# Performance work log

Measured on AMD Instinct MI355X. Metric: run time of the kernel, lower is better.

Reference implementation:

```python
import jax, jax.numpy as jnp
import numpy as np

RATIO = 4

def positional_encoding(d_model, max_len, w_s):
    # w_s: (B,) per-example frequency warp. pe[b, p, 0::2]=sin, pe[b, p, 1::2]=cos
    pos = jnp.arange(max_len, dtype=jnp.float32)                      # (L,)
    div = jnp.power(10000.0, jnp.arange(0, d_model, 2, dtype=jnp.float32) / d_model)  # (d/2,)
    ang = w_s[:, None, None] * pos[None, :, None] / div[None, None, :]  # (B, L, d/2)
    pe = jnp.stack([jnp.sin(ang), jnp.cos(ang)], axis=-1)             # (B, L, d/2, 2)
    return pe.reshape(w_s.shape[0], max_len, d_model)

def setup_inputs() -> dict:
    key = jax.random.key(0)
    ks = jax.random.split(key, 6)
    B, Tds, L, D = 32, 2048, 512, 256
    q = jax.random.normal(ks[0], (B, Tds, D), dtype=jnp.float32)
    k = jax.random.normal(ks[1], (B, L, D), dtype=jnp.float32)
    v = jax.random.normal(ks[2], (B, L, D), dtype=jnp.float32)
    w_compress = jax.random.normal(ks[3], (D // RATIO, D), dtype=jnp.float32) * (D ** -0.5)
    text_lengths = jax.random.randint(ks[4], (B,), L // 2, L + 1).at[0].set(L)
    mel_lengths = jax.random.randint(ks[5], (B,), (Tds * RATIO) // 2, Tds * RATIO + 1).at[0].set(Tds * RATIO)
    return {"q": q, "k": k, "v": v, "w_compress": w_compress,
            "text_lengths": text_lengths, "mel_lengths": mel_lengths}

def reference(q, k, v, w_compress, text_lengths, mel_lengths):
    B, Tds, D = q.shape
    L = k.shape[1]
    # padding masks (True = padded)
    text_mask = jnp.arange(L)[None, :] >= text_lengths[:, None]            # (B, L)
    mel_mask_ds = jnp.arange(Tds)[None, :] >= (mel_lengths // RATIO)[:, None]  # (B, Tds)
    # positional encodings
    q = q + positional_encoding(D, Tds, jnp.ones((B,), dtype=jnp.float32))
    w_s = mel_lengths.astype(jnp.float32) / RATIO / text_lengths.astype(jnp.float32)
    k = k + positional_encoding(D, L, w_s)
    q = q * (float(D) ** -0.5)
    # scores + masked softmax over text axis
    scores = jnp.einsum('btd,bld->btl', q, k)                              # (B, Tds, L)
    scores = jnp.where(text_mask[:, None, :], -jnp.inf, scores)
    align = jax.nn.softmax(scores, axis=-1)
    align = jnp.where(mel_mask_ds[:, :, None], 0.0, align)
    # hard argmax one-hot, straight-through blend
    idx = jnp.argmax(align, axis=-1)                                       # (B, Tds)
    align_oh = jax.nn.one_hot(idx, L, dtype=align.dtype)
    align_oh = jnp.where(mel_mask_ds[:, :, None], 0.0, align_oh)
    blend = align + jax.lax.stop_gradient(align_oh - align)
    attn = jnp.einsum('btl,bld->btd', blend, v)                            # (B, Tds, D)
    # Compress (Linear D -> D//ratio, no bias) then transpose(1,2)
    out = jnp.einsum('btd,cd->bct', attn, w_compress)                      # (B, D//ratio, Tds)
    return out, align
```

## Files before the change

kernel.cpp:

```cpp
#include <hip/hip_runtime.h>
#include <math.h>

#define NB  32
#define TDS 2048
#define LL  512
#define DD  256
#define DC  64
#define GAP_THR 4e-4f

typedef __attribute__((ext_vector_type(8)))  short short8;
typedef __attribute__((ext_vector_type(16))) float f32x16;
typedef __attribute__((ext_vector_type(4)))  float f32x4;

__device__ __forceinline__ unsigned short f2bf(float x) {
    union { float f; unsigned u; } v; v.f = x;
    unsigned r = v.u + 0x7fffu + ((v.u >> 16) & 1u);
    return (unsigned short)(r >> 16);
}
__device__ __forceinline__ float bf2f(unsigned short h) {
    union { unsigned u; float f; } v; v.u = ((unsigned)h) << 16;
    return v.f;
}
__device__ __forceinline__ void gll16(const void* g, void* l) {
    __builtin_amdgcn_global_load_lds(
        (const __attribute__((address_space(1))) void*)g,
        (__attribute__((address_space(3))) void*)l, 16, 0, 0);
}
__device__ __forceinline__ int swz3(int x) { return (x & 7) ^ ((x >> 3) & 7); }


__global__ void peq_kernel(float* __restrict__ peq, int* __restrict__ cnt) {
    int idx = blockIdx.x * 256 + threadIdx.x;
    if (idx == 0) cnt[0] = 0;
    int t = idx >> 8;
    int d = idx & 255;
    int i = d >> 1;
    double invdiv = exp((double)i * (-9.210340371976184 / 128.0));
    double ang = (double)t * invdiv;
    double s, c;
    sincos(ang, &s, &c);
    peq[idx] = (float)((d & 1) ? c : s);
}

__global__ __launch_bounds__(256)
void pek_kernel(const float* __restrict__ k,
                const int* __restrict__ text_lengths,
                const int* __restrict__ mel_lengths,
                char* __restrict__ hi_base,
                char* __restrict__ lo_base) {
    __shared__ double invdiv[128];
    const int tid = threadIdx.x;
    if (tid < 128) invdiv[tid] = exp((double)tid * (-9.210340371976184 / 128.0));
    __syncthreads();
    int f = blockIdx.x * 256 + tid;
    int b = f >> 14;
    int r = f & 16383;
    int ks = r >> 11;
    int rr = r & 2047;
    int lt = rr >> 9;
    int r2 = rr & 511;
    int c  = r2 >> 2;
    int ch = r2 & 3;
    int l  = lt * 128 + c;
    int kk = ks * 32 + ch * 8;
    const float* kr = k + ((size_t)(b * LL + l)) * DD + kk;
    float4 kv0 = *(const float4*)(kr);
    float4 kv1 = *(const float4*)(kr + 4);
    float kv[8] = {kv0.x, kv0.y, kv0.z, kv0.w, kv1.x, kv1.y, kv1.z, kv1.w};
    double wsd = ((double)mel_lengths[b] * 0.25) / (double)text_lengths[b];
    double base_ang = wsd * (double)l;
    unsigned short h[8], lo8[8];
#pragma unroll
    for (int jj = 0; jj < 4; ++jj) {
        int i = (kk >> 1) + jj;
        double ang = base_ang * invdiv[i];
        double n = rint(ang * 0.15915494309189535);
        double red = fma(n, -6.283185307179586, ang);
        float sn, cs;
        sincosf((float)red, &sn, &cs);
        float e0 = kv[2 * jj] + sn;
        float e1 = kv[2 * jj + 1] + cs;
        h[2 * jj]       = f2bf(e0);
        h[2 * jj + 1]   = f2bf(e1);
        lo8[2 * jj]     = f2bf(e0 - bf2f(h[2 * jj]));
        lo8[2 * jj + 1] = f2bf(e1 - bf2f(h[2 * jj + 1]));
    }
    size_t off = (size_t)b * 262144 + (size_t)(ks * 4 + lt) * 8192
               + (size_t)((c * 64 + ch * 16) ^ (swz3(c) << 4));
    uint4 hv, lv;
    hv.x = h[0] | ((unsigned)h[1] << 16); hv.y = h[2] | ((unsigned)h[3] << 16);
    hv.z = h[4] | ((unsigned)h[5] << 16); hv.w = h[6] | ((unsigned)h[7] << 16);
    lv.x = lo8[0] | ((unsigned)lo8[1] << 16); lv.y = lo8[2] | ((unsigned)lo8[3] << 16);
    lv.z = lo8[4] | ((unsigned)lo8[5] << 16); lv.w = lo8[6] | ((unsigned)lo8[7] << 16);
    *(uint4*)(hi_base + off) = hv;
    *(uint4*)(lo_base + off) = lv;
}

__global__ __launch_bounds__(256, 4)
void score_kernel(const float* __restrict__ q,
                  const float* __restrict__ peq,
                  const char* __restrict__ kps_hi,
                  const char* __restrict__ kps_lo,
                  const int* __restrict__ text_lengths,
                  const int* __restrict__ mel_lengths,
                  float* __restrict__ align_out,
                  int* __restrict__ idx_out,
                  int* __restrict__ flag_cnt,
                  int* __restrict__ flags) {
    __shared__ alignas(16) char smB[2 * 16384];
    __shared__ alignas(16) char smA[2 * 4096];

    struct Epi {
        float v1[4][32]; int i1[4][32]; float v2[4][32];
        float S[4][32];  float M[32];
    };
    Epi* ep = (Epi*)smA;

    const int wgid = blockIdx.x;
    const int xcd = wgid & 7, loc = wgid >> 3;
    const int nid = xcd * 256 + loc;
    const int b  = nid >> 6;
    const int t0 = (nid & 63) << 5;

    const int tid = threadIdx.x;
    const int wn = tid >> 6, lane = tid & 63;
    const int c31 = lane & 31, hi5 = lane >> 5;
    const int tlen = text_lengths[b];
    const int melq = mel_lengths[b] >> 2;

    const char* khb = kps_hi + (size_t)b * 262144;
    const char* klb = kps_lo + (size_t)b * 262144;

    f32x16 acc[4];
#pragma unroll
    for (int lt = 0; lt < 4; ++lt)
#pragma unroll
        for (int rg = 0; rg < 16; ++rg) acc[lt][rg] = 0.f;

    const int cB = wn * 32 + c31;
    int aoff[2], boff[2];
#pragma unroll
    for (int kh = 0; kh < 2; ++kh) {
        aoff[kh] = (c31 * 64 + kh * 32 + hi5 * 16) ^ (swz3(c31) << 4);
        boff[kh] = (cB  * 64 + kh * 32 + hi5 * 16) ^ (swz3(cB)  << 4);
    }

    const int sr  = tid >> 3;
    const int sk0 = (tid & 7) * 4;
    const float* qrow = q   + ((size_t)(b * TDS + t0 + sr)) * DD + sk0;
    const float* prow = peq + ((size_t)(t0 + sr)) * DD + sk0;
    const int awaddr = (sr * 64 + sk0 * 2) ^ (swz3(sr) << 4);

#define STAGEB(dbuf, tidx)                                                      \
    {                                                                           \
        const size_t toff = (size_t)(tidx) * 8192 + tid * 16;                   \
        char* dh = smB + (dbuf) * 16384 + tid * 16;                             \
        char* dl = dh + 8192;                                                   \
        gll16(khb + toff, dh); gll16(khb + toff + 4096, dh + 4096);             \
        gll16(klb + toff, dl); gll16(klb + toff + 4096, dl + 4096);             \
    }
#define AWRITE(abufi)                                                           \
    {                                                                           \
        float a0 = (qv4.x + pv4.x) * 0.0625f, a1 = (qv4.y + pv4.y) * 0.0625f;   \
        float a2 = (qv4.z + pv4.z) * 0.0625f, a3 = (qv4.w + pv4.w) * 0.0625f;   \
        unsigned short h0 = f2bf(a0), h1 = f2bf(a1), h2 = f2bf(a2), h3 = f2bf(a3); \
        ushort4 hv = {h0, h1, h2, h3};                                          \
        ushort4 lv = {f2bf(a0 - bf2f(h0)), f2bf(a1 - bf2f(h1)),                 \
                      f2bf(a2 - bf2f(h2)), f2bf(a3 - bf2f(h3))};                \
        *(ushort4*)(smA + (abufi) * 4096 + awaddr) = hv;                        \
        *(ushort4*)(smA + (abufi) * 4096 + 2048 + awaddr) = lv;                 \
    }
#define MFMA6(LT, BUF)                                                          \
    {                                                                           \
        const char* bb = smB + (BUF) * 16384;                                   \
        short8 bh0 = *(const short8*)(bb + boff[0]);                            \
        short8 bl0 = *(const short8*)(bb + 8192 + boff[0]);                     \
        short8 bh1 = *(const short8*)(bb + boff[1]);                            \
        short8 bl1 = *(const short8*)(bb + 8192 + boff[1]);                     \
        acc[LT] = __builtin_amdgcn_mfma_f32_32x32x16_bf16(ah0, bh0, acc[LT], 0, 0, 0); \
        acc[LT] = __builtin_amdgcn_mfma_f32_32x32x16_bf16(ah0, bl0, acc[LT], 0, 0, 0); \
        acc[LT] = __builtin_amdgcn_mfma_f32_32x32x16_bf16(al0, bh0, acc[LT], 0, 0, 0); \
        acc[LT] = __builtin_amdgcn_mfma_f32_32x32x16_bf16(ah1, bh1, acc[LT], 0, 0, 0); \
        acc[LT] = __builtin_amdgcn_mfma_f32_32x32x16_bf16(ah1, bl1, acc[LT], 0, 0, 0); \
        acc[LT] = __builtin_amdgcn_mfma_f32_32x32x16_bf16(al1, bh1, acc[LT], 0, 0, 0); \
    }

    float4 qv4 = *(const float4*)(qrow);
    float4 pv4 = *(const float4*)(prow);
    AWRITE(0)
    STAGEB(0, 0)
    __syncthreads();

    for (int ks = 0; ks < 8; ++ks) {
        const char* abase = smA + (ks & 1) * 4096;
        short8 ah0 = *(const short8*)(abase + aoff[0]);
        short8 ah1 = *(const short8*)(abase + aoff[1]);
        short8 al0 = *(const short8*)(abase + 2048 + aoff[0]);
        short8 al1 = *(const short8*)(abase + 2048 + aoff[1]);
        const int p0 = ks * 4;
        STAGEB(1, p0 + 1)
        MFMA6(0, 0)
        __syncthreads();
        STAGEB(0, p0 + 2)
        if (ks < 7) {
            qv4 = *(const float4*)(qrow + (ks + 1) * 32);
            pv4 = *(const float4*)(prow + (ks + 1) * 32);
        }
        MFMA6(1, 1)
        __syncthreads();
        STAGEB(1, p0 + 3)
        MFMA6(2, 0)
        __syncthreads();
        if (ks < 7) STAGEB(0, p0 + 4)
        MFMA6(3, 1)
        if (ks < 7) AWRITE((ks + 1) & 1)
        __syncthreads();
    }
#undef STAGEB
#undef AWRITE
#undef MFMA6

    const float NEGINF = -__builtin_inff();
#pragma unroll
    for (int lt = 0; lt < 4; ++lt) {
        int col = lt * 128 + cB;
        if (col >= tlen) {
#pragma unroll
            for (int rg = 0; rg < 16; ++rg) acc[lt][rg] = NEGINF;
        }
    }
    float v1[16]; int i1[16]; float v2[16];
#pragma unroll
    for (int rg = 0; rg < 16; ++rg) {
        v1[rg] = acc[0][rg]; i1[rg] = cB; v2[rg] = NEGINF;
#pragma unroll
        for (int lt = 1; lt < 4; ++lt) {
            float v = acc[lt][rg]; int col = lt * 128 + cB;
            if (v > v1[rg]) { v2[rg] = v1[rg]; v1[rg] = v; i1[rg] = col; }
            else if (v > v2[rg]) v2[rg] = v;
        }
    }
#pragma unroll
    for (int off = 1; off <= 16; off <<= 1) {
#pragma unroll
        for (int rg = 0; rg < 16; ++rg) {
            float ov1 = __shfl_xor(v1[rg], off, 64);
            int   oi1 = __shfl_xor(i1[rg], off, 64);
            float ov2 = __shfl_xor(v2[rg], off, 64);
            if (ov1 > v1[rg]) { v2[rg] = fmaxf(v1[rg], ov2); v1[rg] = ov1; i1[rg] = oi1; }
            else if (ov1 < v1[rg]) { v2[rg] = fmaxf(v2[rg], ov1); }
            else { i1[rg] = min(i1[rg], oi1); v2[rg] = v1[rg]; }
        }
    }
    if (c31 == 0) {
#pragma unroll
        for (int rg = 0; rg < 16; ++rg) {
            int r32 = (rg & 3) + 8 * (rg >> 2) + 4 * hi5;
            ep->v1[wn][r32] = v1[rg]; ep->i1[wn][r32] = i1[rg]; ep->v2[wn][r32] = v2[rg];
        }
    }
    __syncthreads();
    {
        const int r32 = c31;
        float V1 = ep->v1[0][r32]; int I1 = ep->i1[0][r32]; float V2 = ep->v2[0][r32];
#pragma unroll
        for (int w = 1; w < 4; ++w) {
            float cv1 = ep->v1[w][r32]; int ci1 = ep->i1[w][r32]; float cv2 = ep->v2[w][r32];
            if (cv1 > V1) { V2 = fmaxf(V1, cv2); V1 = cv1; I1 = ci1; }
            else if (cv1 < V1) { V2 = fmaxf(V2, cv1); }
            else { V2 = V1; }
        }
        if (wn == 0 && hi5 == 0) {
            int t = t0 + r32;
            idx_out[b * TDS + t] = I1;
            if (t < melq && (V1 - V2) < GAP_THR) {
                int pos = atomicAdd(flag_cnt, 1);
                flags[pos] = (b << 11) | t;
            }
            ep->M[r32] = V1;
        }
    }
    __syncthreads();
    float ssum[16];
#pragma unroll
    for (int rg = 0; rg < 16; ++rg) {
        int r32 = (rg & 3) + 8 * (rg >> 2) + 4 * hi5;
        float M = ep->M[r32];
        float s = 0.f;
#pragma unroll
        for (int lt = 0; lt < 4; ++lt) {
            float p = __expf(acc[lt][rg] - M);
            acc[lt][rg] = p; s += p;
        }
        ssum[rg] = s;
    }
#pragma unroll
    for (int off = 1; off <= 16; off <<= 1)
#pragma unroll
        for (int rg = 0; rg < 16; ++rg) ssum[rg] += __shfl_xor(ssum[rg], off, 64);
    if (c31 == 0) {
#pragma unroll
        for (int rg = 0; rg < 16; ++rg) {
            int r32 = (rg & 3) + 8 * (rg >> 2) + 4 * hi5;
            ep->S[wn][r32] = ssum[rg];
        }
    }
    __syncthreads();
#pragma unroll
    for (int rg = 0; rg < 16; ++rg) {
        int r32 = (rg & 3) + 8 * (rg >> 2) + 4 * hi5;
        int t = t0 + r32;
        float denom = ep->S[0][r32] + ep->S[1][r32] + ep->S[2][r32] + ep->S[3][r32];
        float sc = (t < melq) ? (1.0f / denom) : 0.f;
        size_t obase = ((size_t)(b * TDS + t)) * LL + cB;
#pragma unroll
        for (int lt = 0; lt < 4; ++lt)
            __builtin_nontemporal_store(acc[lt][rg] * sc, align_out + obase + lt * 128);
    }
}

__global__ __launch_bounds__(256)
void refine_kernel(const float* __restrict__ q,
                   const float* __restrict__ k,
                   const int* __restrict__ text_lengths,
                   const int* __restrict__ mel_lengths,
                   const int* __restrict__ flags,
                   const int* __restrict__ flag_cnt,
                   int* __restrict__ idx_out) {
    __shared__ double qd[DD];
    __shared__ double invdiv[128];
    __shared__ double rbest[4];
    __shared__ int    ribest[4];
    const int tid = threadIdx.x;
    if (tid < 128)
        invdiv[tid] = 1.0 / pow(10000.0, (double)tid * (1.0 / 128.0));
    const int cnt = flag_cnt[0];
    for (int r = blockIdx.x; r < cnt; r += gridDim.x) {
        const int code = flags[r];
        const int b = code >> 11, t = code & 2047;
        const int tlen = text_lengths[b];
        const double ws = ((double)mel_lengths[b] * 0.25) / (double)text_lengths[b];
        __syncthreads();
        {
            const int d = tid, i = d >> 1;
            double ang = (double)t * invdiv[i];
            double sn, cs;
            sincos(ang, &sn, &cs);
            qd[d] = ((double)q[((size_t)b * TDS + t) * DD + d] + ((d & 1) ? cs : sn)) * 0.0625;
        }
        __syncthreads();
        double best = -1.0e300; int bi = 0x7fffffff;
        for (int p = 0; p < 2; ++p) {
            const int l = tid + p * 256;
            if (l < tlen) {
                const float* kr = k + ((size_t)b * LL + l) * DD;
                const double wl = ws * (double)l;
                double sacc = 0.0;
                for (int i = 0; i < 128; ++i) {
                    double ang = wl * invdiv[i];
                    double sn, cs;
                    sincos(ang, &sn, &cs);
                    sacc += ((double)kr[2 * i]     + sn) * qd[2 * i];
                    sacc += ((double)kr[2 * i + 1] + cs) * qd[2 * i + 1];
                }
                if (sacc > best || (sacc == best && l < bi)) { best = sacc; bi = l; }
            }
        }
        for (int off = 1; off <= 32; off <<= 1) {
            double ov = __shfl_xor(best, off, 64);
            int   oi = __shfl_xor(bi, off, 64);
            if (ov > best || (ov == best && oi < bi)) { best = ov; bi = oi; }
        }
        const int wv = tid >> 6;
        if ((tid & 63) == 0) { rbest[wv] = best; ribest[wv] = bi; }
        __syncthreads();
        if (tid == 0) {
            double bb = rbest[0]; int ii = ribest[0];
            for (int w = 1; w < 4; ++w)
                if (rbest[w] > bb || (rbest[w] == bb && ribest[w] < ii)) { bb = rbest[w]; ii = ribest[w]; }
            idx_out[b * TDS + t] = ii;
        }
    }
}

__global__ __launch_bounds__(256, 4)
void compress_kernel(const float* __restrict__ v,
                     const float* __restrict__ wc,
                     const int* __restrict__ idx_in,
                     const int* __restrict__ mel_lengths,
                     float* __restrict__ out) {
    __shared__ float Ws[256 * 68];
    __shared__ float Vs[16 * 132];
    __shared__ int   idxs[128];
    const int b   = blockIdx.y;
    const int t0  = blockIdx.x * 128;
    const int tid = threadIdx.x;
    const int melq = mel_lengths[b] >> 2;
    const float* vb = v + (size_t)b * LL * DD;

    if (tid < 128) {
        int t = t0 + tid;
        int ii = idx_in[b * TDS + t];
        idxs[tid] = (t >= melq) ? -1 : ii;
    }
#pragma unroll
    for (int r = 0; r < 16; ++r) {
        int f = tid + r * 256;
        int c = f >> 6;
        int u = f & 63;
        float4 wv = *(const float4*)(wc + (size_t)c * DD + u * 4);
        Ws[(u * 4 + 0) * 68 + c] = wv.x;
        Ws[(u * 4 + 1) * 68 + c] = wv.y;
        Ws[(u * 4 + 2) * 68 + c] = wv.z;
        Ws[(u * 4 + 3) * 68 + c] = wv.w;
    }

    const int tx = tid & 7;
    const int ty = tid >> 3;
    const int tv = tid >> 2;
    const int uv = tid & 3;
    float acc[8][4];
#pragma unroll
    for (int i = 0; i < 8; ++i)
#pragma unroll
        for (int j = 0; j < 4; ++j) acc[i][j] = 0.f;

    for (int ks = 0; ks < 16; ++ks) {
        const int d0 = ks * 16;
        __syncthreads();
#pragma unroll
        for (int p = 0; p < 2; ++p) {
            int t = tv + p * 64;
            int row = idxs[t];
            float4 vv = make_float4(0.f, 0.f, 0.f, 0.f);
            if (row >= 0) vv = *(const float4*)(vb + (size_t)row * DD + d0 + uv * 4);
            Vs[(uv * 4 + 0) * 132 + t] = vv.x;
            Vs[(uv * 4 + 1) * 132 + t] = vv.y;
            Vs[(uv * 4 + 2) * 132 + t] = vv.z;
            Vs[(uv * 4 + 3) * 132 + t] = vv.w;
        }
        __syncthreads();
#pragma unroll
        for (int kk = 0; kk < 16; ++kk) {
            const float* wrow = Ws + (size_t)(d0 + kk) * 68 + tx * 8;
            float4 a0 = *(const float4*)(wrow);
            float4 a1 = *(const float4*)(wrow + 4);
            float4 bb = *(const float4*)(Vs + kk * 132 + ty * 4);
            const float av[8] = {a0.x, a0.y, a0.z, a0.w, a1.x, a1.y, a1.z, a1.w};
            const float bv[4] = {bb.x, bb.y, bb.z, bb.w};
#pragma unroll
            for (int i = 0; i < 8; ++i)
#pragma unroll
                for (int j = 0; j < 4; ++j)
                    acc[i][j] = fmaf(av[i], bv[j], acc[i][j]);
        }
    }
#pragma unroll
    for (int ci = 0; ci < 8; ++ci) {
        int c = tx * 8 + ci;
        f32x4 o = {acc[ci][0], acc[ci][1], acc[ci][2], acc[ci][3]};
        __builtin_nontemporal_store(o, (f32x4*)(out + ((size_t)(b * DC + c)) * TDS + t0 + ty * 4));
    }
}

extern "C" void kernel_launch(void* const* d_in, const int* in_sizes, int n_in,
                              void* d_out, int out_size, void* d_ws, size_t ws_size,
                              hipStream_t stream) {
    const float* q    = (const float*)d_in[0];
    const float* k    = (const float*)d_in[1];
    const float* v    = (const float*)d_in[2];
    const float* wc   = (const float*)d_in[3];
    const int*   text = (const int*)d_in[4];
    const int*   mel  = (const int*)d_in[5];

    float* out   = (float*)d_out;
    float* align = out + (size_t)NB * DC * TDS;

    char*  wsb = (char*)d_ws;
    char*  KPS_HI = wsb;
    char*  KPS_LO = wsb + 8388608;
    float* PEQ = (float*)(wsb + 16777216);
    int*   IDX = (int*)(wsb + 16777216 + 2097152);
    int*   CNT = IDX + (size_t)NB * TDS;
    int*   FLG = CNT + 1;

    hipLaunchKernelGGL(peq_kernel, dim3(TDS * DD / 256), dim3(256), 0, stream, PEQ, CNT);
    hipLaunchKernelGGL(pek_kernel, dim3(NB * LL * 32 / 256), dim3(256), 0, stream,
                       k, text, mel, KPS_HI, KPS_LO);
    hipLaunchKernelGGL(score_kernel, dim3(2048), dim3(256), 0, stream,
                       q, PEQ, KPS_HI, KPS_LO, text, mel, align, IDX, CNT, FLG);
    hipLaunchKernelGGL(refine_kernel, dim3(256), dim3(256), 0, stream,
                       q, k, text, mel, FLG, CNT, IDX);
    hipLaunchKernelGGL(compress_kernel, dim3(TDS / 128, NB), dim3(256), 0, stream,
                       v, wc, IDX, mel, out);
}
```

Measured before the change: 232.4 us.

## Load K fragments directly from global in MFMA layout, drop LDS staging

The precomputed K+PE (bf16 hi/lo) buffer is re-laid out so that each lane's MFMA B fragment can be read straight from global memory with 16-byte loads. The score kernel no longer stages K tiles through LDS or hits per-tile barriers, and it register double-buffers the B fragments instead. The whole Q+PE A tile is converted and written to LDS once up front, and each wave now owns a contiguous 128-column slice. This removes LDS traffic and __syncthreads from the main loop, but makes the K reads depend on L2 and raises register pressure.

```diff
diff --git a/kernel.cpp b/kernel.cpp
--- a/kernel.cpp
+++ b/kernel.cpp
@@ -21,12 +21,6 @@
     union { unsigned u; float f; } v; v.u = ((unsigned)h) << 16;
     return v.f;
 }
-__device__ __forceinline__ void gll16(const void* g, void* l) {
-    __builtin_amdgcn_global_load_lds(
-        (const __attribute__((address_space(1))) void*)g,
-        (__attribute__((address_space(3))) void*)l, 16, 0, 0);
-}
-__device__ __forceinline__ int swz3(int x) { return (x & 7) ^ ((x >> 3) & 7); }
 
 
 __global__ void peq_kernel(float* __restrict__ peq, int* __restrict__ cnt) {
@@ -46,8 +40,7 @@
 void pek_kernel(const float* __restrict__ k,
                 const int* __restrict__ text_lengths,
                 const int* __restrict__ mel_lengths,
-                char* __restrict__ hi_base,
-                char* __restrict__ lo_base) {
+                char* __restrict__ kps) {
     __shared__ double invdiv[128];
     const int tid = threadIdx.x;
     if (tid < 128) invdiv[tid] = exp((double)tid * (-9.210340371976184 / 128.0));
@@ -56,14 +49,15 @@
     int b = f >> 14;
     int r = f & 16383;
     int ks = r >> 11;
-    int rr = r & 2047;
-    int lt = rr >> 9;
-    int r2 = rr & 511;
-    int c  = r2 >> 2;
-    int ch = r2 & 3;
-    int l  = lt * 128 + c;
-    int kk = ks * 32 + ch * 8;
-    const float* kr = k + ((size_t)(b * LL + l)) * DD + kk;
+    int r2 = r & 2047;
+    int cs = r2 >> 7;
+    int r3 = r2 & 127;
+    int kh = r3 >> 6;
+    int g  = (r3 >> 5) & 1;
+    int lane32 = r3 & 31;
+    int l  = cs * 32 + lane32;
+    int k0 = ks * 32 + kh * 16 + g * 8;
+    const float* kr = k + ((size_t)(b * LL + l)) * DD + k0;
     float4 kv0 = *(const float4*)(kr);
     float4 kv1 = *(const float4*)(kr + 4);
     float kv[8] = {kv0.x, kv0.y, kv0.z, kv0.w, kv1.x, kv1.y, kv1.z, kv1.w};
@@ -72,49 +66,46 @@
     unsigned short h[8], lo8[8];
 #pragma unroll
     for (int jj = 0; jj < 4; ++jj) {
-        int i = (kk >> 1) + jj;
+        int i = (k0 >> 1) + jj;
         double ang = base_ang * invdiv[i];
         double n = rint(ang * 0.15915494309189535);
         double red = fma(n, -6.283185307179586, ang);
-        float sn, cs;
-        sincosf((float)red, &sn, &cs);
+        float sn, cs2;
+        sincosf((float)red, &sn, &cs2);
         float e0 = kv[2 * jj] + sn;
-        float e1 = kv[2 * jj + 1] + cs;
+        float e1 = kv[2 * jj + 1] + cs2;
         h[2 * jj]       = f2bf(e0);
         h[2 * jj + 1]   = f2bf(e1);
         lo8[2 * jj]     = f2bf(e0 - bf2f(h[2 * jj]));
         lo8[2 * jj + 1] = f2bf(e1 - bf2f(h[2 * jj + 1]));
     }
-    size_t off = (size_t)b * 262144 + (size_t)(ks * 4 + lt) * 8192
-               + (size_t)((c * 64 + ch * 16) ^ (swz3(c) << 4));
+    size_t off = (size_t)b * 524288 + (size_t)ks * 65536 + (size_t)cs * 4096
+               + kh * 1024 + g * 512 + lane32 * 16;
     uint4 hv, lv;
     hv.x = h[0] | ((unsigned)h[1] << 16); hv.y = h[2] | ((unsigned)h[3] << 16);
     hv.z = h[4] | ((unsigned)h[5] << 16); hv.w = h[6] | ((unsigned)h[7] << 16);
     lv.x = lo8[0] | ((unsigned)lo8[1] << 16); lv.y = lo8[2] | ((unsigned)lo8[3] << 16);
     lv.z = lo8[4] | ((unsigned)lo8[5] << 16); lv.w = lo8[6] | ((unsigned)lo8[7] << 16);
-    *(uint4*)(hi_base + off) = hv;
-    *(uint4*)(lo_base + off) = lv;
+    *(uint4*)(kps + off) = hv;
+    *(uint4*)(kps + off + 2048) = lv;
 }
 
 __global__ __launch_bounds__(256, 4)
 void score_kernel(const float* __restrict__ q,
                   const float* __restrict__ peq,
-                  const char* __restrict__ kps_hi,
-                  const char* __restrict__ kps_lo,
+                  const char* __restrict__ kps,
                   const int* __restrict__ text_lengths,
                   const int* __restrict__ mel_lengths,
                   float* __restrict__ align_out,
                   int* __restrict__ idx_out,
                   int* __restrict__ flag_cnt,
                   int* __restrict__ flags) {
-    __shared__ alignas(16) char smB[2 * 16384];
-    __shared__ alignas(16) char smA[2 * 4096];
-
+    __shared__ alignas(16) char smA[32768];
     struct Epi {
         float v1[4][32]; int i1[4][32]; float v2[4][32];
         float S[4][32];  float M[32];
     };
-    Epi* ep = (Epi*)smA;
+    __shared__ Epi ep;
 
     const int wgid = blockIdx.x;
     const int xcd = wgid & 7, loc = wgid >> 3;
@@ -128,114 +119,104 @@
     const int tlen = text_lengths[b];
     const int melq = mel_lengths[b] >> 2;
 
-    const char* khb = kps_hi + (size_t)b * 262144;
-    const char* klb = kps_lo + (size_t)b * 262144;
+    const char* kpb = kps + (size_t)b * 524288 + (size_t)(hi5 * 512 + c31 * 16);
 
     f32x16 acc[4];
 #pragma unroll
-    for (int lt = 0; lt < 4; ++lt)
-#pragma unroll
-        for (int rg = 0; rg < 16; ++rg) acc[lt][rg] = 0.f;
-
-    const int cB = wn * 32 + c31;
-    int aoff[2], boff[2];
-#pragma unroll
-    for (int kh = 0; kh < 2; ++kh) {
-        aoff[kh] = (c31 * 64 + kh * 32 + hi5 * 16) ^ (swz3(c31) << 4);
-        boff[kh] = (cB  * 64 + kh * 32 + hi5 * 16) ^ (swz3(cB)  << 4);
-    }
-
-    const int sr  = tid >> 3;
-    const int sk0 = (tid & 7) * 4;
-    const float* qrow = q   + ((size_t)(b * TDS + t0 + sr)) * DD + sk0;
-    const float* prow = peq + ((size_t)(t0 + sr)) * DD + sk0;
-    const int awaddr = (sr * 64 + sk0 * 2) ^ (swz3(sr) << 4);
-
-#define STAGEB(dbuf, tidx)                                                      \
+    for (int ci = 0; ci < 4; ++ci)
+#pragma unroll
+        for (int rg = 0; rg < 16; ++rg) acc[ci][rg] = 0.f;
+
+#define BLOAD(dst, ksv, civ)                                                    \
     {                                                                           \
-        const size_t toff = (size_t)(tidx) * 8192 + tid * 16;                   \
-        char* dh = smB + (dbuf) * 16384 + tid * 16;                             \
-        char* dl = dh + 8192;                                                   \
-        gll16(khb + toff, dh); gll16(khb + toff + 4096, dh + 4096);             \
-        gll16(klb + toff, dl); gll16(klb + toff + 4096, dl + 4096);             \
-    }
-#define AWRITE(abufi)                                                           \
+        const char* p = kpb + (ksv) * 65536 + (wn * 4 + (civ)) * 4096;          \
+        dst[0] = *(const short8*)(p);                                           \
+        dst[1] = *(const short8*)(p + 1024);                                    \
+        dst[2] = *(const short8*)(p + 2048);                                    \
+        dst[3] = *(const short8*)(p + 3072);                                    \
+    }
+#define MFMA6(CI, B)                                                            \
     {                                                                           \
-        float a0 = (qv4.x + pv4.x) * 0.0625f, a1 = (qv4.y + pv4.y) * 0.0625f;   \
-        float a2 = (qv4.z + pv4.z) * 0.0625f, a3 = (qv4.w + pv4.w) * 0.0625f;   \
-        unsigned short h0 = f2bf(a0), h1 = f2bf(a1), h2 = f2bf(a2), h3 = f2bf(a3); \
-        ushort4 hv = {h0, h1, h2, h3};                                          \
-        ushort4 lv = {f2bf(a0 - bf2f(h0)), f2bf(a1 - bf2f(h1)),                 \
-                      f2bf(a2 - bf2f(h2)), f2bf(a3 - bf2f(h3))};                \
-        *(ushort4*)(smA + (abufi) * 4096 + awaddr) = hv;                        \
-        *(ushort4*)(smA + (abufi) * 4096 + 2048 + awaddr) = lv;                 \
-    }
-#define MFMA6(LT, BUF)                                                          \
-    {                                                                           \
-        const char* bb = smB + (BUF) * 16384;                                   \
-        short8 bh0 = *(const short8*)(bb + boff[0]);                            \
-        short8 bl0 = *(const short8*)(bb + 8192 + boff[0]);                     \
-        short8 bh1 = *(const short8*)(bb + boff[1]);                            \
-        short8 bl1 = *(const short8*)(bb + 8192 + boff[1]);                     \
-        acc[LT] = __builtin_amdgcn_mfma_f32_32x32x16_bf16(ah0, bh0, acc[LT], 0, 0, 0); \
-        acc[LT] = __builtin_amdgcn_mfma_f32_32x32x16_bf16(ah0, bl0, acc[LT], 0, 0, 0); \
-        acc[LT] = __builtin_amdgcn_mfma_f32_32x32x16_bf16(al0, bh0, acc[LT], 0, 0, 0); \
-        acc[LT] = __builtin_amdgcn_mfma_f32_32x32x16_bf16(ah1, bh1, acc[LT], 0, 0, 0); \
-        acc[LT] = __builtin_amdgcn_mfma_f32_32x32x16_bf16(ah1, bl1, acc[LT], 0, 0, 0); \
-        acc[LT] = __builtin_amdgcn_mfma_f32_32x32x16_bf16(al1, bh1, acc[LT], 0, 0, 0); \
-    }
-
-    float4 qv4 = *(const float4*)(qrow);
-    float4 pv4 = *(const float4*)(prow);
-    AWRITE(0)
-    STAGEB(0, 0)
+        acc[CI] = __builtin_amdgcn_mfma_f32_32x32x16_bf16(ah0, B[0], acc[CI], 0, 0, 0); \
+        acc[CI] = __builtin_amdgcn_mfma_f32_32x32x16_bf16(ah0, B[2], acc[CI], 0, 0, 0); \
+        acc[CI] = __builtin_amdgcn_mfma_f32_32x32x16_bf16(al0, B[0], acc[CI], 0, 0, 0); \
+        acc[CI] = __builtin_amdgcn_mfma_f32_32x32x16_bf16(ah1, B[1], acc[CI], 0, 0, 0); \
+        acc[CI] = __builtin_amdgcn_mfma_f32_32x32x16_bf16(ah1, B[3], acc[CI], 0, 0, 0); \
+        acc[CI] = __builtin_amdgcn_mfma_f32_32x32x16_bf16(al1, B[1], acc[CI], 0, 0, 0); \
+    }
+
+    short8 B0[4], B1[4];
+    BLOAD(B0, 0, 0)
+
+    {
+        const int sr = tid >> 3, kc = tid & 7;
+        const float* qr = q   + ((size_t)(b * TDS) + t0 + sr) * DD;
+        const float* pr = peq + (size_t)(t0 + sr) * DD;
+#pragma unroll
+        for (int kq = 0; kq < 4; ++kq) {
+            int m = kq * 8 + kc;
+            int k0 = m * 8;
+            float4 qa = *(const float4*)(qr + k0);
+            float4 qb4 = *(const float4*)(qr + k0 + 4);
+            float4 pa = *(const float4*)(pr + k0);
+            float4 pb = *(const float4*)(pr + k0 + 4);
+            float e[8] = {(qa.x + pa.x) * 0.0625f, (qa.y + pa.y) * 0.0625f,
+                          (qa.z + pa.z) * 0.0625f, (qa.w + pa.w) * 0.0625f,
+                          (qb4.x + pb.x) * 0.0625f, (qb4.y + pb.y) * 0.0625f,
+                          (qb4.z + pb.z) * 0.0625f, (qb4.w + pb.w) * 0.0625f};
+            unsigned short h[8], lo[8];
+#pragma unroll
+            for (int j = 0; j < 8; ++j) {
+                h[j] = f2bf(e[j]);
+                lo[j] = f2bf(e[j] - bf2f(h[j]));
+            }
+            uint4 hv, lv;
+            hv.x = h[0] | ((unsigned)h[1] << 16); hv.y = h[2] | ((unsigned)h[3] << 16);
+            hv.z = h[4] | ((unsigned)h[5] << 16); hv.w = h[6] | ((unsigned)h[7] << 16);
+            lv.x = lo[0] | ((unsigned)lo[1] << 16); lv.y = lo[2] | ((unsigned)lo[3] << 16);
+            lv.z = lo[4] | ((unsigned)lo[5] << 16); lv.w = lo[6] | ((unsigned)lo[7] << 16);
+            int base = (m >> 2) * 4096 + ((m >> 1) & 1) * 1024 + (m & 1) * 512 + sr * 16;
+            *(uint4*)(smA + base) = hv;
+            *(uint4*)(smA + base + 2048) = lv;
+        }
+    }
     __syncthreads();
 
+    const int afr = hi5 * 512 + c31 * 16;
     for (int ks = 0; ks < 8; ++ks) {
-        const char* abase = smA + (ks & 1) * 4096;
-        short8 ah0 = *(const short8*)(abase + aoff[0]);
-        short8 ah1 = *(const short8*)(abase + aoff[1]);
-        short8 al0 = *(const short8*)(abase + 2048 + aoff[0]);
-        short8 al1 = *(const short8*)(abase + 2048 + aoff[1]);
-        const int p0 = ks * 4;
-        STAGEB(1, p0 + 1)
-        MFMA6(0, 0)
-        __syncthreads();
-        STAGEB(0, p0 + 2)
-        if (ks < 7) {
-            qv4 = *(const float4*)(qrow + (ks + 1) * 32);
-            pv4 = *(const float4*)(prow + (ks + 1) * 32);
-        }
-        MFMA6(1, 1)
-        __syncthreads();
-        STAGEB(1, p0 + 3)
-        MFMA6(2, 0)
-        __syncthreads();
-        if (ks < 7) STAGEB(0, p0 + 4)
-        MFMA6(3, 1)
-        if (ks < 7) AWRITE((ks + 1) & 1)
-        __syncthreads();
-    }
-#undef STAGEB
-#undef AWRITE
+        const char* ab = smA + ks * 4096 + afr;
+        short8 ah0 = *(const short8*)(ab);
+        short8 ah1 = *(const short8*)(ab + 1024);
+        short8 al0 = *(const short8*)(ab + 2048);
+        short8 al1 = *(const short8*)(ab + 3072);
+        BLOAD(B1, ks, 1)
+        MFMA6(0, B0)
+        BLOAD(B0, ks, 2)
+        MFMA6(1, B1)
+        BLOAD(B1, ks, 3)
+        MFMA6(2, B0)
+        if (ks < 7) BLOAD(B0, ks + 1, 0)
+        MFMA6(3, B1)
+    }
+#undef BLOAD
 #undef MFMA6
 
     const float NEGINF = -__builtin_inff();
 #pragma unroll
-    for (int lt = 0; lt < 4; ++lt) {
-        int col = lt * 128 + cB;
+    for (int ci = 0; ci < 4; ++ci) {
+        int col = wn * 128 + ci * 32 + c31;
         if (col >= tlen) {
 #pragma unroll
-            for (int rg = 0; rg < 16; ++rg) acc[lt][rg] = NEGINF;
+            for (int rg = 0; rg < 16; ++rg) acc[ci][rg] = NEGINF;
         }
     }
     float v1[16]; int i1[16]; float v2[16];
 #pragma unroll
     for (int rg = 0; rg < 16; ++rg) {
-        v1[rg] = acc[0][rg]; i1[rg] = cB; v2[rg] = NEGINF;
-#pragma unroll
-        for (int lt = 1; lt < 4; ++lt) {
-            float v = acc[lt][rg]; int col = lt * 128 + cB;
+        v1[rg] = acc[0][rg]; i1[rg] = wn * 128 + c31; v2[rg] = NEGINF;
+#pragma unroll
+        for (int ci = 1; ci < 4; ++ci) {
+            float v = acc[ci][rg]; int col = wn * 128 + ci * 32 + c31;
             if (v > v1[rg]) { v2[rg] = v1[rg]; v1[rg] = v; i1[rg] = col; }
             else if (v > v2[rg]) v2[rg] = v;
         }
@@ -256,16 +237,16 @@
 #pragma unroll
         for (int rg = 0; rg < 16; ++rg) {
             int r32 = (rg & 3) + 8 * (rg >> 2) + 4 * hi5;
-            ep->v1[wn][r32] = v1[rg]; ep->i1[wn][r32] = i1[rg]; ep->v2[wn][r32] = v2[rg];
+            ep.v1[wn][r32] = v1[rg]; ep.i1[wn][r32] = i1[rg]; ep.v2[wn][r32] = v2[rg];
         }
     }
     __syncthreads();
     {
         const int r32 = c31;
-        float V1 = ep->v1[0][r32]; int I1 = ep->i1[0][r32]; float V2 = ep->v2[0][r32];
+        float V1 = ep.v1[0][r32]; int I1 = ep.i1[0][r32]; float V2 = ep.v2[0][r32];
 #pragma unroll
         for (int w = 1; w < 4; ++w) {
-            float cv1 = ep->v1[w][r32]; int ci1 = ep->i1[w][r32]; float cv2 = ep->v2[w][r32];
+            float cv1 = ep.v1[w][r32]; int ci1 = ep.i1[w][r32]; float cv2 = ep.v2[w][r32];
             if (cv1 > V1) { V2 = fmaxf(V1, cv2); V1 = cv1; I1 = ci1; }
             else if (cv1 < V1) { V2 = fmaxf(V2, cv1); }
             else { V2 = V1; }
@@ -277,7 +258,7 @@
                 int pos = atomicAdd(flag_cnt, 1);
                 flags[pos] = (b << 11) | t;
             }
-            ep->M[r32] = V1;
+            ep.M[r32] = V1;
         }
     }
     __syncthreads();
@@ -285,12 +266,12 @@
 #pragma unroll
     for (int rg = 0; rg < 16; ++rg) {
         int r32 = (rg & 3) + 8 * (rg >> 2) + 4 * hi5;
-        float M = ep->M[r32];
+        float M = ep.M[r32];
         float s = 0.f;
 #pragma unroll
-        for (int lt = 0; lt < 4; ++lt) {
-            float p = __expf(acc[lt][rg] - M);
-            acc[lt][rg] = p; s += p;
+        for (int ci = 0; ci < 4; ++ci) {
+            float p = __expf(acc[ci][rg] - M);
+            acc[ci][rg] = p; s += p;
         }
         ssum[rg] = s;
     }
@@ -302,7 +283,7 @@
 #pragma unroll
         for (int rg = 0; rg < 16; ++rg) {
             int r32 = (rg & 3) + 8 * (rg >> 2) + 4 * hi5;
-            ep->S[wn][r32] = ssum[rg];
+            ep.S[wn][r32] = ssum[rg];
         }
     }
     __syncthreads();
@@ -310,12 +291,12 @@
     for (int rg = 0; rg < 16; ++rg) {
         int r32 = (rg & 3) + 8 * (rg >> 2) + 4 * hi5;
         int t = t0 + r32;
-        float denom = ep->S[0][r32] + ep->S[1][r32] + ep->S[2][r32] + ep->S[3][r32];
+        float denom = ep.S[0][r32] + ep.S[1][r32] + ep.S[2][r32] + ep.S[3][r32];
         float sc = (t < melq) ? (1.0f / denom) : 0.f;
-        size_t obase = ((size_t)(b * TDS + t)) * LL + cB;
-#pragma unroll
-        for (int lt = 0; lt < 4; ++lt)
-            __builtin_nontemporal_store(acc[lt][rg] * sc, align_out + obase + lt * 128);
+        size_t obase = ((size_t)(b * TDS + t)) * LL + wn * 128 + c31;
+#pragma unroll
+        for (int ci = 0; ci < 4; ++ci)
+            __builtin_nontemporal_store(acc[ci][rg] * sc, align_out + obase + ci * 32);
     }
 }
 
@@ -477,18 +458,17 @@
     float* align = out + (size_t)NB * DC * TDS;
 
     char*  wsb = (char*)d_ws;
-    char*  KPS_HI = wsb;
-    char*  KPS_LO = wsb + 8388608;
+    char*  KPS = wsb;
     float* PEQ = (float*)(wsb + 16777216);
     int*   IDX = (int*)(wsb + 16777216 + 2097152);
     int*   CNT = IDX + (size_t)NB * TDS;
     int*   FLG = CNT + 1;
 
     hipLaunchKernelGGL(peq_kernel, dim3(TDS * DD / 256), dim3(256), 0, stream, PEQ, CNT);
-    hipLaunchKernelGGL(pek_kernel, dim3(NB * LL * 32 / 256), dim3(256), 0, stream,
-                       k, text, mel, KPS_HI, KPS_LO);
+    hipLaunchKernelGGL(pek_kernel, dim3(NB * 16384 / 256), dim3(256), 0, stream,
+                       k, text, mel, KPS);
     hipLaunchKernelGGL(score_kernel, dim3(2048), dim3(256), 0, stream,
-                       q, PEQ, KPS_HI, KPS_LO, text, mel, align, IDX, CNT, FLG);
+                       q, PEQ, KPS, text, mel, align, IDX, CNT, FLG);
     hipLaunchKernelGGL(refine_kernel, dim3(256), dim3(256), 0, stream,
                        q, k, text, mel, FLG, CNT, IDX);
     hipLaunchKernelGGL(compress_kernel, dim3(TDS / 128, NB), dim3(256), 0, stream,
```

Result: faster. 223.4 us (-3.9%).
